# Performance work log

Measured on AMD Instinct MI355X. Metric: run time of the kernel, lower is better.

The kernel has to match this reference:

```python
import jax, jax.numpy as jnp
import numpy as np

NUM_EMBEDDINGS = 512
EMBEDDING_DIM = 64
COMMITMENT_COST = 0.25


def setup_inputs() -> dict:
    key = jax.random.key(0)
    k_in, k_emb = jax.random.split(key)
    inputs = jax.random.normal(k_in, (8, EMBEDDING_DIM, 16, 32, 32), dtype=jnp.float32)
    # nn.Embedding weight initialized uniform(-1/K, 1/K)
    bound = 1.0 / NUM_EMBEDDINGS
    embedding = jax.random.uniform(
        k_emb, (NUM_EMBEDDINGS, EMBEDDING_DIM), dtype=jnp.float32,
        minval=-bound, maxval=bound)
    return {"inputs": inputs, "embedding": embedding}


def reference(inputs, embedding):
    B, C, T, H, W = inputs.shape  # C == embedding_dim
    # (B, C, T, H, W) -> (B, T, H, W, C) -> (N, C)
    inputs_perm = jnp.transpose(inputs, (0, 2, 3, 4, 1))
    flat = inputs_perm.reshape(-1, C)  # [N, D]
    # squared euclidean distances to each codebook vector: [N, K]
    distances = (jnp.sum(flat ** 2, axis=1, keepdims=True)
                 + jnp.sum(embedding ** 2, axis=1)
                 - 2.0 * jnp.matmul(flat, embedding.T))
    encoding_indices = jnp.argmin(distances, axis=1)  # [N]
    indices_reshaped = encoding_indices.reshape(B, T, H, W)
    # gather codebook vectors and restore (B, C, T, H, W)
    quantized = embedding[encoding_indices].reshape(B, T, H, W, C)
    quantized = jnp.transpose(quantized, (0, 4, 1, 2, 3))
    # losses (stop-gradient structure preserved for faithfulness)
    e_latent_loss = jnp.mean((jax.lax.stop_gradient(quantized) - inputs) ** 2)
    q_latent_loss = jnp.mean((quantized - jax.lax.stop_gradient(inputs)) ** 2)
    loss = q_latent_loss + COMMITMENT_COST * e_latent_loss
    # straight-through estimator
    quantized_st = inputs + jax.lax.stop_gradient(quantized - inputs)
    return (quantized_st, loss, indices_reshaped)
```

## Files before the change

### kernel.cpp

```cpp
#include <hip/hip_runtime.h>

#define SPATIAL   16384
#define DIM       64
#define KCODES    512
#define NPOS      131072
#define QST_ELEMS 8388608
#define LOSS_OFF  8388608
#define IDX_OFF   8388609
#define KTILE     256
#define NKTILES   (KCODES / KTILE)
#define NBLOCKS   (NPOS / 256)

__device__ __forceinline__ float mul_rn(float a, float b) {
#pragma clang fp contract(off)
    return a * b;
}
__device__ __forceinline__ float add_rn(float a, float b) {
#pragma clang fp contract(off)
    return a + b;
}
__device__ __forceinline__ float sub_rn(float a, float b) {
#pragma clang fp contract(off)
    return a - b;
}

__device__ __forceinline__ float np_sumsq64(const float* v) {
    float r[8];
#pragma unroll
    for (int j = 0; j < 8; ++j) r[j] = mul_rn(v[j], v[j]);
#pragma unroll
    for (int i = 8; i < 64; i += 8) {
#pragma unroll
        for (int j = 0; j < 8; ++j) r[j] = add_rn(r[j], mul_rn(v[i + j], v[i + j]));
    }
    return add_rn(add_rn(add_rn(r[0], r[1]), add_rn(r[2], r[3])),
                  add_rn(add_rn(r[4], r[5]), add_rn(r[6], r[7])));
}

__global__ void vq_e2_kernel(const float* __restrict__ emb, float* __restrict__ e2) {
    int k = threadIdx.x;
    if (k >= KCODES) return;
    float v[DIM];
#pragma unroll
    for (int d = 0; d < DIM; ++d) v[d] = emb[k * DIM + d];
    e2[k] = np_sumsq64(v);
}

#define DECLX float4 x0,x1,x2q,x3,x4,x5,x6,x7,x8,x9,x10,x11,x12,x13,x14,x15;

#define LOADX(v,q) \
    v.x = xin[(size_t)(4*(q)+0)*SPATIAL]; \
    v.y = xin[(size_t)(4*(q)+1)*SPATIAL]; \
    v.z = xin[(size_t)(4*(q)+2)*SPATIAL]; \
    v.w = xin[(size_t)(4*(q)+3)*SPATIAL];

#define SQA(ve,vo) \
    r0 = add_rn(r0, mul_rn(ve.x, ve.x)); r1 = add_rn(r1, mul_rn(ve.y, ve.y)); \
    r2 = add_rn(r2, mul_rn(ve.z, ve.z)); r3 = add_rn(r3, mul_rn(ve.w, ve.w)); \
    r4 = add_rn(r4, mul_rn(vo.x, vo.x)); r5 = add_rn(r5, mul_rn(vo.y, vo.y)); \
    r6 = add_rn(r6, mul_rn(vo.z, vo.z)); r7 = add_rn(r7, mul_rn(vo.w, vo.w));

#define DSTEP(v,q) { \
    float4 ea = era[q], eb = erb[q]; \
    acca = __builtin_fmaf(v.x, ea.x, acca); accb = __builtin_fmaf(v.x, eb.x, accb); \
    acca = __builtin_fmaf(v.y, ea.y, acca); accb = __builtin_fmaf(v.y, eb.y, accb); \
    acca = __builtin_fmaf(v.z, ea.z, acca); accb = __builtin_fmaf(v.z, eb.z, accb); \
    acca = __builtin_fmaf(v.w, ea.w, acca); accb = __builtin_fmaf(v.w, eb.w, accb); }

#define EPIQ(v,q) { \
    float4 e4 = eq4[q]; \
    float dd; \
    dd = sub_rn(e4.x, v.x); oq[(size_t)(4*(q)+0)*SPATIAL] = add_rn(v.x, dd); lsum += (double)mul_rn(dd, dd); \
    dd = sub_rn(e4.y, v.y); oq[(size_t)(4*(q)+1)*SPATIAL] = add_rn(v.y, dd); lsum += (double)mul_rn(dd, dd); \
    dd = sub_rn(e4.z, v.z); oq[(size_t)(4*(q)+2)*SPATIAL] = add_rn(v.z, dd); lsum += (double)mul_rn(dd, dd); \
    dd = sub_rn(e4.w, v.w); oq[(size_t)(4*(q)+3)*SPATIAL] = add_rn(v.w, dd); lsum += (double)mul_rn(dd, dd); }

__global__ __launch_bounds__(256, 2) void vq_main_kernel(
        const float* __restrict__ in, const float* __restrict__ emb,
        const float* __restrict__ e2, float* __restrict__ out,
        double* __restrict__ losspart) {
    __shared__ float4 sev[KTILE * DIM / 4];
    __shared__ float  se2[KTILE];
    __shared__ double lpart[4];

    const int t = threadIdx.x;
    const int p = blockIdx.x * 256 + t;
    const int b = p >> 14;
    const int s = p & 16383;
    const float* xin = in + (size_t)b * (DIM * SPATIAL) + s;

    DECLX
    LOADX(x0, 0)  LOADX(x1, 1)  LOADX(x2q, 2) LOADX(x3, 3)
    LOADX(x4, 4)  LOADX(x5, 5)  LOADX(x6, 6)  LOADX(x7, 7)
    LOADX(x8, 8)  LOADX(x9, 9)  LOADX(x10,10) LOADX(x11,11)
    LOADX(x12,12) LOADX(x13,13) LOADX(x14,14) LOADX(x15,15)

    float r0 = mul_rn(x0.x, x0.x), r1 = mul_rn(x0.y, x0.y);
    float r2 = mul_rn(x0.z, x0.z), r3 = mul_rn(x0.w, x0.w);
    float r4 = mul_rn(x1.x, x1.x), r5 = mul_rn(x1.y, x1.y);
    float r6 = mul_rn(x1.z, x1.z), r7 = mul_rn(x1.w, x1.w);
    SQA(x2q, x3) SQA(x4, x5) SQA(x6, x7) SQA(x8, x9)
    SQA(x10, x11) SQA(x12, x13) SQA(x14, x15)
    const float x2 = add_rn(add_rn(add_rn(r0, r1), add_rn(r2, r3)),
                            add_rn(add_rn(r4, r5), add_rn(r6, r7)));

    float best = __builtin_inff();
    int bidx = 0;

    for (int tile = 0; tile < NKTILES; ++tile) {
        const float4* esrc = (const float4*)(emb + (size_t)tile * KTILE * DIM);
#pragma unroll
        for (int i = 0; i < 16; ++i) sev[t + i * 256] = esrc[t + i * 256];
        if (t < KTILE / 4) ((float4*)se2)[t] = ((const float4*)(e2 + tile * KTILE))[t];
        __syncthreads();

        const int kbase = tile * KTILE;
        for (int kk = 0; kk < KTILE; kk += 2) {
            const float4* era = sev + (size_t)kk * (DIM / 4);
            const float4* erb = era + (DIM / 4);
            float acca = 0.0f, accb = 0.0f;
            DSTEP(x0, 0)  DSTEP(x1, 1)  DSTEP(x2q, 2) DSTEP(x3, 3)
            DSTEP(x4, 4)  DSTEP(x5, 5)  DSTEP(x6, 6)  DSTEP(x7, 7)
            DSTEP(x8, 8)  DSTEP(x9, 9)  DSTEP(x10,10) DSTEP(x11,11)
            DSTEP(x12,12) DSTEP(x13,13) DSTEP(x14,14) DSTEP(x15,15)
            float twoa = mul_rn(2.0f, acca);
            float twob = mul_rn(2.0f, accb);
            float dista = sub_rn(add_rn(x2, se2[kk]),     twoa);
            float distb = sub_rn(add_rn(x2, se2[kk + 1]), twob);
            if (dista < best) { best = dista; bidx = kbase + kk; }
            if (distb < best) { best = distb; bidx = kbase + kk + 1; }
        }
        __syncthreads();
    }

    out[IDX_OFF + p] = (float)bidx;

    const float4* eq4 = (const float4*)(emb + (size_t)bidx * DIM);
    float* oq = out + (size_t)b * (DIM * SPATIAL) + s;
    double lsum = 0.0;
    EPIQ(x0, 0)  EPIQ(x1, 1)  EPIQ(x2q, 2) EPIQ(x3, 3)
    EPIQ(x4, 4)  EPIQ(x5, 5)  EPIQ(x6, 6)  EPIQ(x7, 7)
    EPIQ(x8, 8)  EPIQ(x9, 9)  EPIQ(x10,10) EPIQ(x11,11)
    EPIQ(x12,12) EPIQ(x13,13) EPIQ(x14,14) EPIQ(x15,15)

#pragma unroll
    for (int off = 32; off > 0; off >>= 1) lsum += __shfl_down(lsum, off, 64);
    const int lane = t & 63, wave = t >> 6;
    if (lane == 0) lpart[wave] = lsum;
    __syncthreads();
    if (t == 0) losspart[blockIdx.x] = ((lpart[0] + lpart[1]) + lpart[2]) + lpart[3];
}

__global__ void vq_finalize_kernel(const double* __restrict__ part,
                                   float* __restrict__ out) {
    __shared__ double sdata[256];
    int t = threadIdx.x;
    sdata[t] = part[t] + part[t + 256];
    __syncthreads();
    for (int stride = 128; stride > 0; stride >>= 1) {
        if (t < stride) sdata[t] = sdata[t] + sdata[t + stride];
        __syncthreads();
    }
    if (t == 0) {
        double m = sdata[0] / (double)QST_ELEMS;
        float mf = (float)m;
        out[LOSS_OFF] = add_rn(mf, mul_rn(0.25f, mf));
    }
}

extern "C" void kernel_launch(void* const* d_in, const int* in_sizes, int n_in,
                              void* d_out, int out_size, void* d_ws, size_t ws_size,
                              hipStream_t stream) {
    const float* in  = (const float*)d_in[0];
    const float* emb = (const float*)d_in[1];
    float* out = (float*)d_out;
    double* losspart = (double*)d_ws;
    float* e2 = (float*)((char*)d_ws + NBLOCKS * sizeof(double));

    vq_e2_kernel<<<1, KCODES, 0, stream>>>(emb, e2);
    vq_main_kernel<<<NBLOCKS, 256, 0, stream>>>(in, emb, e2, out, losspart);
    vq_finalize_kernel<<<1, 256, 0, stream>>>(losspart, out);
}
```

Baseline: 157.2 us.

## Split codebook search across two waves per position, read codebook directly from global

Each block now handles 64 positions with two waves, and each wave scans half of the codebook for the same positions. The two partial argmins are merged through shared memory, and the epilogue stores are split between the waves. The shared-memory codebook staging and its barriers are dropped in favour of wave-uniform global/scalar loads of codebook rows. This doubles parallelism, with more blocks and shorter serial loops per thread, in exchange for reloading each input position in both waves and relying on scalar cache bandwidth for codebook reads.

New measurement: 580.1 us. 3.69x slower.

```diff
diff --git a/kernel.cpp b/kernel.cpp
--- a/kernel.cpp
+++ b/kernel.cpp
@@ -7,9 +7,10 @@
 #define QST_ELEMS 8388608
 #define LOSS_OFF  8388608
 #define IDX_OFF   8388609
-#define KTILE     256
-#define NKTILES   (KCODES / KTILE)
-#define NBLOCKS   (NPOS / 256)
+
+#define POSB      64
+#define NBLOCKS   (NPOS / POSB)
+#define KPW       (KCODES / 2)
 
 __device__ __forceinline__ float mul_rn(float a, float b) {
 #pragma clang fp contract(off)
@@ -60,12 +61,11 @@
     r4 = add_rn(r4, mul_rn(vo.x, vo.x)); r5 = add_rn(r5, mul_rn(vo.y, vo.y)); \
     r6 = add_rn(r6, mul_rn(vo.z, vo.z)); r7 = add_rn(r7, mul_rn(vo.w, vo.w));
 
-#define DSTEP(v,q) { \
-    float4 ea = era[q], eb = erb[q]; \
-    acca = __builtin_fmaf(v.x, ea.x, acca); accb = __builtin_fmaf(v.x, eb.x, accb); \
-    acca = __builtin_fmaf(v.y, ea.y, acca); accb = __builtin_fmaf(v.y, eb.y, accb); \
-    acca = __builtin_fmaf(v.z, ea.z, acca); accb = __builtin_fmaf(v.z, eb.z, accb); \
-    acca = __builtin_fmaf(v.w, ea.w, acca); accb = __builtin_fmaf(v.w, eb.w, accb); }
+#define DSTEPS(v,q) { \
+    acc = __builtin_fmaf(v.x, ek[4*(q)+0], acc); \
+    acc = __builtin_fmaf(v.y, ek[4*(q)+1], acc); \
+    acc = __builtin_fmaf(v.z, ek[4*(q)+2], acc); \
+    acc = __builtin_fmaf(v.w, ek[4*(q)+3], acc); }
 
 #define EPIQ(v,q) { \
     float4 e4 = eq4[q]; \
@@ -75,16 +75,18 @@
     dd = sub_rn(e4.z, v.z); oq[(size_t)(4*(q)+2)*SPATIAL] = add_rn(v.z, dd); lsum += (double)mul_rn(dd, dd); \
     dd = sub_rn(e4.w, v.w); oq[(size_t)(4*(q)+3)*SPATIAL] = add_rn(v.w, dd); lsum += (double)mul_rn(dd, dd); }
 
-__global__ __launch_bounds__(256, 2) void vq_main_kernel(
+__global__ __launch_bounds__(128, 4) void vq_main_kernel(
         const float* __restrict__ in, const float* __restrict__ emb,
         const float* __restrict__ e2, float* __restrict__ out,
         double* __restrict__ losspart) {
-    __shared__ float4 sev[KTILE * DIM / 4];
-    __shared__ float  se2[KTILE];
-    __shared__ double lpart[4];
+    __shared__ float  sbest[2][POSB];
+    __shared__ int    sidx[2][POSB];
+    __shared__ double lpart[2];
 
     const int t = threadIdx.x;
-    const int p = blockIdx.x * 256 + t;
+    const int lane = t & 63;
+    const int wave = t >> 6;
+    const int p = blockIdx.x * POSB + lane;
     const int b = p >> 14;
     const int s = p & 16383;
     const float* xin = in + (size_t)b * (DIM * SPATIAL) + s;
@@ -104,58 +106,61 @@
     const float x2 = add_rn(add_rn(add_rn(r0, r1), add_rn(r2, r3)),
                             add_rn(add_rn(r4, r5), add_rn(r6, r7)));
 
+    const int kstart = wave * KPW;
     float best = __builtin_inff();
-    int bidx = 0;
-
-    for (int tile = 0; tile < NKTILES; ++tile) {
-        const float4* esrc = (const float4*)(emb + (size_t)tile * KTILE * DIM);
-#pragma unroll
-        for (int i = 0; i < 16; ++i) sev[t + i * 256] = esrc[t + i * 256];
-        if (t < KTILE / 4) ((float4*)se2)[t] = ((const float4*)(e2 + tile * KTILE))[t];
-        __syncthreads();
-
-        const int kbase = tile * KTILE;
-        for (int kk = 0; kk < KTILE; kk += 2) {
-            const float4* era = sev + (size_t)kk * (DIM / 4);
-            const float4* erb = era + (DIM / 4);
-            float acca = 0.0f, accb = 0.0f;
-            DSTEP(x0, 0)  DSTEP(x1, 1)  DSTEP(x2q, 2) DSTEP(x3, 3)
-            DSTEP(x4, 4)  DSTEP(x5, 5)  DSTEP(x6, 6)  DSTEP(x7, 7)
-            DSTEP(x8, 8)  DSTEP(x9, 9)  DSTEP(x10,10) DSTEP(x11,11)
-            DSTEP(x12,12) DSTEP(x13,13) DSTEP(x14,14) DSTEP(x15,15)
-            float twoa = mul_rn(2.0f, acca);
-            float twob = mul_rn(2.0f, accb);
-            float dista = sub_rn(add_rn(x2, se2[kk]),     twoa);
-            float distb = sub_rn(add_rn(x2, se2[kk + 1]), twob);
-            if (dista < best) { best = dista; bidx = kbase + kk; }
-            if (distb < best) { best = distb; bidx = kbase + kk + 1; }
-        }
-        __syncthreads();
+    int bidx = kstart;
+#pragma unroll 2
+    for (int kk = 0; kk < KPW; ++kk) {
+        const int k = kstart + kk;
+        const float* ek = emb + (size_t)k * DIM;
+        float acc = 0.0f;
+        DSTEPS(x0, 0)  DSTEPS(x1, 1)  DSTEPS(x2q, 2) DSTEPS(x3, 3)
+        DSTEPS(x4, 4)  DSTEPS(x5, 5)  DSTEPS(x6, 6)  DSTEPS(x7, 7)
+        DSTEPS(x8, 8)  DSTEPS(x9, 9)  DSTEPS(x10,10) DSTEPS(x11,11)
+        DSTEPS(x12,12) DSTEPS(x13,13) DSTEPS(x14,14) DSTEPS(x15,15)
+        float dist = sub_rn(add_rn(x2, e2[k]), mul_rn(2.0f, acc));
+        if (dist < best) { best = dist; bidx = k; }
     }
 
-    out[IDX_OFF + p] = (float)bidx;
+    sbest[wave][lane] = best;
+    sidx[wave][lane]  = bidx;
+    __syncthreads();
+    float fb = sbest[0][lane];
+    int   fi = sidx[0][lane];
+    {
+        float dv = sbest[1][lane];
+        int   iv = sidx[1][lane];
+        if (dv < fb) { fb = dv; fi = iv; }
+    }
 
-    const float4* eq4 = (const float4*)(emb + (size_t)bidx * DIM);
+    if (wave == 0) out[IDX_OFF + p] = (float)fi;
+
+    const float4* eq4 = (const float4*)(emb + (size_t)fi * DIM);
     float* oq = out + (size_t)b * (DIM * SPATIAL) + s;
     double lsum = 0.0;
-    EPIQ(x0, 0)  EPIQ(x1, 1)  EPIQ(x2q, 2) EPIQ(x3, 3)
-    EPIQ(x4, 4)  EPIQ(x5, 5)  EPIQ(x6, 6)  EPIQ(x7, 7)
-    EPIQ(x8, 8)  EPIQ(x9, 9)  EPIQ(x10,10) EPIQ(x11,11)
-    EPIQ(x12,12) EPIQ(x13,13) EPIQ(x14,14) EPIQ(x15,15)
+    if (wave == 0) {
+        EPIQ(x0, 0) EPIQ(x1, 1) EPIQ(x2q, 2) EPIQ(x3, 3)
+        EPIQ(x4, 4) EPIQ(x5, 5) EPIQ(x6, 6)  EPIQ(x7, 7)
+    } else {
+        EPIQ(x8, 8)   EPIQ(x9, 9)   EPIQ(x10, 10) EPIQ(x11, 11)
+        EPIQ(x12, 12) EPIQ(x13, 13) EPIQ(x14, 14) EPIQ(x15, 15)
+    }
 
 #pragma unroll
     for (int off = 32; off > 0; off >>= 1) lsum += __shfl_down(lsum, off, 64);
-    const int lane = t & 63, wave = t >> 6;
     if (lane == 0) lpart[wave] = lsum;
     __syncthreads();
-    if (t == 0) losspart[blockIdx.x] = ((lpart[0] + lpart[1]) + lpart[2]) + lpart[3];
+    if (t == 0) losspart[blockIdx.x] = lpart[0] + lpart[1];
 }
 
 __global__ void vq_finalize_kernel(const double* __restrict__ part,
                                    float* __restrict__ out) {
     __shared__ double sdata[256];
     int t = threadIdx.x;
-    sdata[t] = part[t] + part[t + 256];
+    double a = 0.0;
+#pragma unroll
+    for (int i = 0; i < NBLOCKS / 256; ++i) a += part[t + 256 * i];
+    sdata[t] = a;
     __syncthreads();
     for (int stride = 128; stride > 0; stride >>= 1) {
         if (t < stride) sdata[t] = sdata[t] + sdata[t + stride];
@@ -178,6 +183,6 @@
     float* e2 = (float*)((char*)d_ws + NBLOCKS * sizeof(double));
 
     vq_e2_kernel<<<1, KCODES, 0, stream>>>(emb, e2);
-    vq_main_kernel<<<NBLOCKS, 256, 0, stream>>>(in, emb, e2, out, losspart);
+    vq_main_kernel<<<NBLOCKS, 128, 0, stream>>>(in, emb, e2, out, losspart);
     vq_finalize_kernel<<<1, 256, 0, stream>>>(losspart, out);
 }
```
